# Performance work log

Hardware: AMD Instinct MI355X
Metric: run time of the kernel (lower is better)

## Reference

```python
import jax, jax.numpy as jnp
import numpy as np
from math import sqrt

B, L, H, D = 4, 4096, 8, 64
FACTOR = 5


def setup_inputs():
    key = jax.random.key(0)
    k1, k2, k3, k4 = jax.random.split(key, 4)
    queries = jax.random.normal(k1, (B, L, H, D), dtype=jnp.float32)
    keys = jax.random.normal(k2, (B, L, H, D), dtype=jnp.float32)
    values = jax.random.normal(k3, (B, L, H, D), dtype=jnp.float32)
    sample_k = min(FACTOR * int(np.ceil(np.log(L))), L)  # U_part = 45
    index_sample = jax.random.randint(k4, (L, sample_k), 0, L)
    return {"queries": queries, "keys": keys, "values": values,
            "index_sample": index_sample}


def reference(queries, keys, values, index_sample):
    Bq, L_Q, Hq, Dq = queries.shape
    L_K = keys.shape[1]
    Q = jnp.transpose(queries, (0, 2, 1, 3))  # [B,H,L_Q,D]
    K = jnp.transpose(keys, (0, 2, 1, 3))     # [B,H,L_K,D]
    V = jnp.transpose(values, (0, 2, 1, 3))   # [B,H,L_K,D]
    n_top = min(FACTOR * int(np.ceil(np.log(L_Q))), L_Q)  # u = 45

    # --- _prob_QK: randomly-sampled QK scoring + top-k query selection ---
    K_sample = K[:, :, index_sample, :]                       # [B,H,L_Q,sample_k,D]
    Q_K_sample = jnp.einsum('bhld,bhlkd->bhlk', Q, K_sample)  # [B,H,L_Q,sample_k]
    M = Q_K_sample.max(-1) - Q_K_sample.sum(-1) / L_K         # sparsity measure
    _, M_top = jax.lax.top_k(M, n_top)                        # [B,H,u] query indices
    Q_reduce = jnp.take_along_axis(Q, M_top[..., None], axis=2)  # [B,H,u,D]
    scores = jnp.einsum('bhud,bhkd->bhuk', Q_reduce, K)       # [B,H,u,L_K]

    # scale = 1/sqrt(D) (self.scale is None)
    scores = scores * (1.0 / sqrt(Dq))

    # --- ProbMask (mask_flag=True): causal, key j masked if j > query idx ---
    mask = jnp.arange(L_K)[None, None, None, :] > M_top[..., None]
    scores = jnp.where(mask, -jnp.inf, scores)
    attn = jax.nn.softmax(scores, axis=-1)                    # [B,H,u,L_K]

    # --- initial context (masked case): cumulative sum of V over time ---
    context = jnp.cumsum(V, axis=2)                           # [B,H,L_Q,D]

    # --- scatter attn@V into the selected query positions ---
    upd = jnp.einsum('bhuk,bhkd->bhud', attn, V)              # [B,H,u,D]
    b_idx = jnp.arange(Bq)[:, None, None]
    h_idx = jnp.arange(Hq)[None, :, None]
    context = context.at[b_idx, h_idx, M_top].set(upd)
    return context  # [B,H,L_Q,D], as returned by the torch module
```

## Files before the change

### kernel.cpp

```cpp
#include <hip/hip_runtime.h>

#define NB 4
#define LSEQ 4096
#define NH 8
#define ND 64
#define NSAMP 45
#define NTOP 45
#define ACH 256
#define NCH (LSEQ / ACH)

typedef float f32x4 __attribute__((ext_vector_type(4)));


__global__ __launch_bounds__(256) void fusedA_kernel(
        const int* __restrict__ idxS, int* __restrict__ sortedPack,
        const float* __restrict__ V, float* __restrict__ chunkSums) {
    int blk = blockIdx.x;
    int t = threadIdx.x;
    __shared__ int cnt[256][17];
    __shared__ float part[4][ND];

    if (blk < 16) {
        int l = blk * 256 + t;
        const int* is = idxS + (size_t)l * NSAMP;
        #pragma unroll
        for (int c = 0; c < 16; ++c) cnt[t][c] = 0;
        for (int s = 0; s < NSAMP; ++s) cnt[t][is[s] >> 8] += 1;
        int run = 0;
        #pragma unroll
        for (int c = 0; c < 16; ++c) { int v = cnt[t][c]; cnt[t][c] = run; run += v; }
        for (int s = 0; s < NSAMP; ++s) {
            int idx = is[s];
            int pos = cnt[t][idx >> 8]++;
            sortedPack[(size_t)l * NSAMP + pos] = (idx << 8) | s;
        }
    } else {
        int blk2 = blk - 16;
        int c = blk2 & 15;
        int bh = blk2 >> 4;
        int h = bh & (NH - 1);
        int b = bh >> 3;
        int g = t >> 6, d = t & 63;

        const size_t rstride = (size_t)NH * ND;
        size_t vbase = (size_t)b * LSEQ * rstride + (size_t)h * ND + d;

        int l0 = c * 256 + g * 64;
        float s = 0.0f;
        for (int l = l0; l < l0 + 64; ++l) s += V[vbase + (size_t)l * rstride];

        part[g][d] = s;
        __syncthreads();
        if (t < ND)
            chunkSums[(size_t)blk2 * ND + d] =
                part[0][d] + part[1][d] + part[2][d] + part[3][d];
    }
}

__global__ __launch_bounds__(512, 1) void compute_M_kernel(
        const float* __restrict__ Q,
        const float* __restrict__ K,
        const int* __restrict__ sortedPack,
        float* __restrict__ Mout) {
    int xcd = blockIdx.x & 7;
    int sub = blockIdx.x >> 3;
    int bh  = (xcd << 2) | (sub & 3);
    int lt  = sub >> 2;
    int b = bh >> 3, h = bh & 7;
    int t = threadIdx.x;
    int l0 = (lt << 9) + t;

    __shared__ float Ks[256 * 68];
    __shared__ float Plds[512 * 45];

    f32x4 qa[16];
    {
        const f32x4* qp0 = reinterpret_cast<const f32x4*>(
            Q + (((size_t)b * LSEQ + l0) * NH + h) * ND);
        #pragma unroll
        for (int i = 0; i < 16; ++i) qa[i] = __builtin_nontemporal_load(qp0 + i);
    }

    auto dotQK = [&](const f32x4 (&q4)[16], const float* kr) -> float {
        const f32x4* k4 = reinterpret_cast<const f32x4*>(kr);
        float w[32];
        #pragma unroll
        for (int i = 0; i < 8; ++i) {
            f32x4 a = q4[i], bb = k4[i], c = q4[i + 8], d4 = k4[i + 8];
            w[4 * i + 0] = __fadd_rn(__fmul_rn(a.x, bb.x), __fmul_rn(c.x, d4.x));
            w[4 * i + 1] = __fadd_rn(__fmul_rn(a.y, bb.y), __fmul_rn(c.y, d4.y));
            w[4 * i + 2] = __fadd_rn(__fmul_rn(a.z, bb.z), __fmul_rn(c.z, d4.z));
            w[4 * i + 3] = __fadd_rn(__fmul_rn(a.w, bb.w), __fmul_rn(c.w, d4.w));
        }
        #pragma unroll
        for (int off = 16; off; off >>= 1) {
            #pragma unroll
            for (int i = 0; i < off; ++i) w[i] = __fadd_rn(w[i], w[i + off]);
        }
        return w[0];
    };

    const int* sp0 = sortedPack + (size_t)l0 * NSAMP;
    int ptr0 = 0;
    int pk0 = sp0[0];

    size_t kbh = ((size_t)b * LSEQ * NH + h) * ND;

    for (int c = 0; c < 16; ++c) {
        #pragma unroll
        for (int i = 0; i < 8; ++i) {
            int flat = i * 512 + t;
            int row = flat >> 4, col = flat & 15;
            f32x4 v = *reinterpret_cast<const f32x4*>(
                K + kbh + (size_t)(c * 256 + row) * (NH * ND) + col * 4);
            *reinterpret_cast<f32x4*>(&Ks[row * 68 + col * 4]) = v;
        }
        __syncthreads();

        while ((pk0 >> 16) == c) {
            int r = (pk0 >> 8) & 255;
            int s = pk0 & 255;
            Plds[t * 45 + s] = dotQK(qa, &Ks[r * 68]);
            ++ptr0;
            pk0 = (ptr0 < NSAMP) ? sp0[ptr0] : 0x7fffffff;
        }
        __syncthreads();
    }

    {
        float maxv = -INFINITY, sumv = 0.0f;
        for (int s = 0; s < NSAMP; ++s) {
            float v = Plds[t * 45 + s];
            maxv = fmaxf(maxv, v);
            sumv = __fadd_rn(sumv, v);
        }
        Mout[(size_t)bh * LSEQ + l0] = maxv - sumv * (1.0f / (float)LSEQ);
    }
}

__global__ __launch_bounds__(256) void topk_kernel(
        const float* __restrict__ M, int* __restrict__ Mtop) {
    int bh = blockIdx.x;
    int t = threadIdx.x;
    int wave = t >> 6, lane = t & 63;
    const float* m = M + (size_t)bh * LSEQ;

    float rv[16];
    #pragma unroll
    for (int k = 0; k < 16; ++k) rv[k] = m[t + (k << 8)];

    __shared__ float wv[4];
    __shared__ int   wi[4];
    __shared__ int   winIdx;

    for (int iter = 0; iter < NTOP; ++iter) {
        float bv = -INFINITY; int bi = 0x7fffffff;
        #pragma unroll
        for (int k = 0; k < 16; ++k) {
            float v = rv[k];
            if (v > bv) { bv = v; bi = t + (k << 8); }
        }
        #pragma unroll
        for (int off = 1; off < 64; off <<= 1) {
            float ov = __shfl_xor(bv, off, 64);
            int   oi = __shfl_xor(bi, off, 64);
            if (ov > bv || (ov == bv && oi < bi)) { bv = ov; bi = oi; }
        }
        if (lane == 0) { wv[wave] = bv; wi[wave] = bi; }
        __syncthreads();
        if (t == 0) {
            float cv = wv[0]; int ci = wi[0];
            for (int ww = 1; ww < 4; ++ww) {
                if (wv[ww] > cv || (wv[ww] == cv && wi[ww] < ci)) { cv = wv[ww]; ci = wi[ww]; }
            }
            winIdx = ci;
            Mtop[bh * NTOP + iter] = ci;
        }
        __syncthreads();
        int widx = winIdx;
        #pragma unroll
        for (int k = 0; k < 16; ++k)
            if (widx == t + (k << 8)) rv[k] = -INFINITY;
        __syncthreads();
    }
}

__global__ __launch_bounds__(256, 1) void attn_partial_kernel(
        const float* __restrict__ Q, const float* __restrict__ K,
        const float* __restrict__ V, const int* __restrict__ Mtop,
        float* __restrict__ part) {
    int bh = blockIdx.x >> 4;
    int c  = blockIdx.x & 15;
    int b = bh >> 3, h = bh & 7;
    int t = threadIdx.x;
    int w = t >> 6, lane = t & 63;
    int jj = lane >> 4, dq = lane & 15;

    __shared__ float Qs[NTOP * ND];
    __shared__ int   posS[NTOP];
    __shared__ float Vs[64][68];
    __shared__ float Pw[4][64];

    size_t base = ((size_t)b * LSEQ * NH + h) * ND;

    if (t < NTOP) posS[t] = Mtop[bh * NTOP + t];
    __syncthreads();
    for (int idx = t; idx < NTOP * 16; idx += 256) {
        int u = idx >> 4, cg = idx & 15;
        f32x4 v = *reinterpret_cast<const f32x4*>(
            Q + base + (size_t)posS[u] * (NH * ND) + cg * 4);
        *reinterpret_cast<f32x4*>(&Qs[u * ND + cg * 4]) = v;
    }

    f32x4 o[12];
    float mreg[12], sreg[12];
    #pragma unroll
    for (int qi = 0; qi < 12; ++qi) {
        o[qi] = 0.0f; mreg[qi] = -INFINITY; sreg[qi] = 0.0f;
    }

    for (int tt = 0; tt < ACH / 64; ++tt) {
        int tile0 = c * ACH + tt * 64;
        __syncthreads();
        #pragma unroll
        for (int i = 0; i < 4; ++i) {
            int flat = i * 256 + t;
            int r = flat >> 4, cg = flat & 15;
            f32x4 v = *reinterpret_cast<const f32x4*>(
                V + base + (size_t)(tile0 + r) * (NH * ND) + cg * 4);
            *reinterpret_cast<f32x4*>(&Vs[r][cg * 4]) = v;
        }
        __syncthreads();

        f32x4 kreg[16];
        #pragma unroll
        for (int i = 0; i < 16; ++i)
            kreg[i] = *reinterpret_cast<const f32x4*>(
                K + base + (size_t)(tile0 + lane) * (NH * ND) + i * 4);

        #pragma unroll
        for (int qi = 0; qi < 12; ++qi) {
            int u = w + 4 * qi;
            if (u >= NTOP) continue;
            int pu = posS[u];
            if (pu < tile0) continue;

            float a0 = 0, a1 = 0, a2 = 0, a3 = 0;
            #pragma unroll
            for (int di = 0; di < 16; ++di) {
                f32x4 qv = *reinterpret_cast<const f32x4*>(&Qs[u * ND + di * 4]);
                a0 = fmaf(qv.x, kreg[di].x, a0);
                a1 = fmaf(qv.y, kreg[di].y, a1);
                a2 = fmaf(qv.z, kreg[di].z, a2);
                a3 = fmaf(qv.w, kreg[di].w, a3);
            }
            float sc = ((a0 + a1) + (a2 + a3)) * 0.125f;
            if (tile0 + lane > pu) sc = -INFINITY;

            float tmax = sc;
            #pragma unroll
            for (int off = 1; off < 64; off <<= 1)
                tmax = fmaxf(tmax, __shfl_xor(tmax, off, 64));
            float mold = mreg[qi];
            float mnew = fmaxf(mold, tmax);
            float alpha = __expf(mold - mnew);
            float e = __expf(sc - mnew);
            float esum = e;
            #pragma unroll
            for (int off = 1; off < 64; off <<= 1)
                esum += __shfl_xor(esum, off, 64);
            sreg[qi] = sreg[qi] * alpha + esum;
            mreg[qi] = mnew;
            Pw[w][lane] = e;
            o[qi] *= alpha;
            #pragma unroll
            for (int i = 0; i < 16; ++i) {
                float pe = Pw[w][i * 4 + jj];
                f32x4 vv = *reinterpret_cast<const f32x4*>(&Vs[i * 4 + jj][dq * 4]);
                o[qi] += vv * pe;
            }
        }
    }

    #pragma unroll
    for (int qi = 0; qi < 12; ++qi) {
        int u = w + 4 * qi;
        if (u >= NTOP) continue;
        if (posS[u] < c * ACH) continue;
        f32x4 oo = o[qi];
        #pragma unroll
        for (int off = 16; off <= 32; off <<= 1) {
            oo.x += __shfl_xor(oo.x, off, 64);
            oo.y += __shfl_xor(oo.y, off, 64);
            oo.z += __shfl_xor(oo.z, off, 64);
            oo.w += __shfl_xor(oo.w, off, 64);
        }
        size_t pb = ((size_t)(bh * NTOP + u) * NCH + c) * 72;
        if (lane < 16)
            *reinterpret_cast<f32x4*>(&part[pb + 4 + dq * 4]) = oo;
        if (lane == 0) { part[pb] = mreg[qi]; part[pb + 1] = sreg[qi]; }
    }
}

__global__ __launch_bounds__(256) void attn_merge_kernel(
        const float* __restrict__ part, const int* __restrict__ Mtop,
        float* __restrict__ ctx) {
    int j = blockIdx.x * 4 + (threadIdx.x >> 6);
    int lane = threadIdx.x & 63;
    int bh = j / NTOP, u = j - bh * NTOP;
    int pos = Mtop[bh * NTOP + u];
    int cmax = pos >> 8;
    size_t pb0 = (size_t)(bh * NTOP + u) * NCH * 72;
    float m = -INFINITY;
    for (int cc = 0; cc <= cmax; ++cc)
        m = fmaxf(m, part[pb0 + (size_t)cc * 72]);
    float S = 0.0f, oacc = 0.0f;
    for (int cc = 0; cc <= cmax; ++cc) {
        float mc = part[pb0 + (size_t)cc * 72];
        float sc = part[pb0 + (size_t)cc * 72 + 1];
        float wgt = __expf(mc - m);
        S = fmaf(sc, wgt, S);
        oacc = fmaf(part[pb0 + (size_t)cc * 72 + 4 + lane], wgt, oacc);
    }
    ctx[(size_t)j * ND + lane] = oacc / S;
}

__global__ __launch_bounds__(256) void cumsumCS_kernel(
        const float* __restrict__ V, const float* __restrict__ chunkSums,
        const int* __restrict__ Mtop, const float* __restrict__ ctx,
        float* __restrict__ out, int doScatter) {
    int blk = blockIdx.x;
    int c = blk & 15;
    int bh = blk >> 4;
    int h = bh & (NH - 1);
    int b = bh >> 3;
    int g = threadIdx.x >> 6, d = threadIdx.x & 63;
    int t = threadIdx.x;

    const size_t rstride = (size_t)NH * ND;
    size_t vbase = (size_t)b * LSEQ * rstride + (size_t)h * ND + d;

    float run = 0.0f;
    for (int cc = 0; cc < c; ++cc)
        run += chunkSums[((size_t)bh * 16 + cc) * ND + d];

    int l0 = c * 256 + g * 64;
    float s = 0.0f;
    for (int l = l0; l < l0 + 64; ++l) s += V[vbase + (size_t)l * rstride];
    __shared__ float part[4][ND];
    part[g][d] = s;
    __syncthreads();
    for (int gg = 0; gg < g; ++gg) run += part[gg][d];

    size_t obase = (size_t)bh * LSEQ * ND + d;
    for (int l = l0; l < l0 + 64; ++l) {
        run += V[vbase + (size_t)l * rstride];
        out[obase + (size_t)l * ND] = run;
    }

    if (!doScatter) return;
    __syncthreads();
    for (int idx = t; idx < NTOP * ND; idx += 256) {
        int u = idx >> 6, d2 = idx & 63;
        int pos = Mtop[bh * NTOP + u];
        if ((pos >> 8) == c)
            out[((size_t)bh * LSEQ + pos) * ND + d2] =
                ctx[(size_t)(bh * NTOP + u) * ND + d2];
    }
}

#define TJ 64
__global__ __launch_bounds__(256) void attn_rows_kernel(
        const float* __restrict__ Q,
        const float* __restrict__ K,
        const float* __restrict__ V,
        const int* __restrict__ Mtop,
        float* __restrict__ out) {
    int x = blockIdx.x;
    int xcd = x & 7;
    int slot = x >> 3;
    int grp = slot / NTOP;
    int u = slot % NTOP;
    int bh = grp * 8 + xcd;
    int h = bh & (NH - 1);
    int b = bh >> 3;
    int pos = Mtop[bh * NTOP + u];
    int n = pos + 1;
    int t = threadIdx.x;
    int r = t >> 2, qt = t & 3;

    __shared__ float Ks[TJ][65];
    __shared__ float Vs[TJ][65];
    __shared__ float red[256];

    const size_t rstride = (size_t)NH * ND;
    size_t base = (size_t)b * LSEQ * rstride + (size_t)h * ND;

    float qreg[16];
    const float* qrow = Q + base + (size_t)pos * rstride + qt * 16;
    #pragma unroll
    for (int i = 0; i < 16; i += 4) {
        float4 v4 = *reinterpret_cast<const float4*>(qrow + i);
        qreg[i] = v4.x; qreg[i + 1] = v4.y; qreg[i + 2] = v4.z; qreg[i + 3] = v4.w;
    }

    float m = -INFINITY, s = 0.0f;
    float o[16];
    #pragma unroll
    for (int dd = 0; dd < 16; ++dd) o[dd] = 0.0f;

    int ntiles = (n + TJ - 1) / TJ;
    for (int tt = 0; tt < ntiles; ++tt) {
        int j0 = tt * TJ;
        __syncthreads();
        #pragma unroll
        for (int i = 0; i < 4; ++i) {
            int u16 = t + i * 256;
            int rr = u16 >> 4, cc = u16 & 15;
            int j = j0 + rr;
            int jc = (j < n) ? j : (n - 1);
            const float* rowk = K + base + (size_t)jc * rstride;
            float4 kv = *reinterpret_cast<const float4*>(rowk + cc * 4);
            Ks[rr][cc * 4 + 0] = kv.x; Ks[rr][cc * 4 + 1] = kv.y;
            Ks[rr][cc * 4 + 2] = kv.z; Ks[rr][cc * 4 + 3] = kv.w;
            const float* rowv = V + base + (size_t)jc * rstride;
            float4 vv = *reinterpret_cast<const float4*>(rowv + cc * 4);
            Vs[rr][cc * 4 + 0] = vv.x; Vs[rr][cc * 4 + 1] = vv.y;
            Vs[rr][cc * 4 + 2] = vv.z; Vs[rr][cc * 4 + 3] = vv.w;
        }
        __syncthreads();

        int j = j0 + r;
        float acc = 0.0f;
        #pragma unroll
        for (int dd = 0; dd < 16; ++dd)
            acc = fmaf(qreg[dd], Ks[r][qt * 16 + dd], acc);
        acc += __shfl_xor(acc, 1, 64);
        acc += __shfl_xor(acc, 2, 64);

        if (j < n) {
            float sc = acc * 0.125f;
            if (sc > m) {
                float alpha = __expf(m - sc);
                s *= alpha;
                #pragma unroll
                for (int dd = 0; dd < 16; ++dd) o[dd] *= alpha;
                m = sc;
            }
            float e = __expf(sc - m);
            s += e;
            #pragma unroll
            for (int dd = 0; dd < 16; ++dd)
                o[dd] = fmaf(e, Vs[r][qt * 16 + dd], o[dd]);
        }
    }
    __syncthreads();

    red[t] = m; __syncthreads();
    for (int sft = 128; sft; sft >>= 1) {
        if (t < sft) red[t] = fmaxf(red[t], red[t + sft]);
        __syncthreads();
    }
    float mstar = red[0]; __syncthreads();
    float a = __expf(m - mstar);

    red[t] = s * a; __syncthreads();
    for (int sft = 128; sft; sft >>= 1) {
        if (t < sft) red[t] += red[t + sft];
        __syncthreads();
    }
    float S = red[0]; __syncthreads();

    float* OB = &Ks[0][0];
    #pragma unroll
    for (int dd = 0; dd < 16; ++dd) OB[t * 16 + dd] = o[dd] * a;
    __syncthreads();

    if (t < ND) {
        int qtt = t >> 4, dd = t & 15;
        float tot = 0.0f;
        for (int k = 0; k < 64; ++k) tot += OB[(4 * k + qtt) * 16 + dd];
        out[((size_t)bh * LSEQ + pos) * ND + t] = tot / S;
    }
}

extern "C" void kernel_launch(void* const* d_in, const int* in_sizes, int n_in,
                              void* d_out, int out_size, void* d_ws, size_t ws_size,
                              hipStream_t stream) {
    const float* Q = (const float*)d_in[0];
    const float* K = (const float*)d_in[1];
    const float* V = (const float*)d_in[2];
    const int* idxS = (const int*)d_in[3];
    float* out = (float*)d_out;

    float* Mbuf = (float*)d_out;
    int*   sortedPack = (int*)((char*)d_out + (1 << 20));
    float* part = (float*)((char*)d_out + (2 << 20));
    int*   Mtop = (int*)d_ws;
    float* chunkSums = (float*)((char*)d_ws + 8192);
    float* ctx = (float*)((char*)d_ws + 8192 + 131072);
    size_t wsMid = 8192 + 131072 + (size_t)NB * NH * NTOP * ND * 4;

    fusedA_kernel<<<528, 256, 0, stream>>>(idxS, sortedPack, V, chunkSums);
    compute_M_kernel<<<256, 512, 0, stream>>>(Q, K, sortedPack, Mbuf);
    topk_kernel<<<NB * NH, 256, 0, stream>>>(Mbuf, Mtop);

    if (ws_size >= wsMid) {
        attn_partial_kernel<<<NB * NH * NCH, 256, 0, stream>>>(Q, K, V, Mtop, part);
        attn_merge_kernel<<<NB * NH * NTOP / 4, 256, 0, stream>>>(part, Mtop, ctx);
        cumsumCS_kernel<<<NB * NH * 16, 256, 0, stream>>>(V, chunkSums, Mtop, ctx, out, 1);
    } else {
        cumsumCS_kernel<<<NB * NH * 16, 256, 0, stream>>>(V, chunkSums, Mtop, ctx, out, 0);
        attn_rows_kernel<<<NB * NH * NTOP, 256, 0, stream>>>(Q, K, V, Mtop, out);
    }
}
```

Before: 424.3 us.

## Split sample dots across 1024 threads and fuse attention merge into cumsum scatter

compute_M now runs 1024 threads per block: two threads per query, each handling an interleaved half of the sorted sample list. It stages K in 512-row tiles and keeps a running max and sum in registers instead of writing every dot product to LDS, then combines the two halves through shared memory. The separate merge kernel is removed, and the scatter step of the cumsum kernel now merges the per-chunk softmax partials directly, which drops one launch and the ctx round trip. The partials buffer moves into the workspace, so the fast path now needs a much larger workspace; if it is not available, the slower row-wise fallback runs.

```diff
diff --git a/kernel.cpp b/kernel.cpp
--- a/kernel.cpp
+++ b/kernel.cpp
@@ -8,12 +8,13 @@
 #define NTOP 45
 #define ACH 256
 #define NCH (LSEQ / ACH)
+#define SENT 0x7fffffff
 
 typedef float f32x4 __attribute__((ext_vector_type(4)));
 
 
 __global__ __launch_bounds__(256) void fusedA_kernel(
-        const int* __restrict__ idxS, int* __restrict__ sortedPack,
+        const int* __restrict__ idxS, int* __restrict__ sortedAB,
         const float* __restrict__ V, float* __restrict__ chunkSums) {
     int blk = blockIdx.x;
     int t = threadIdx.x;
@@ -29,10 +30,12 @@
         int run = 0;
         #pragma unroll
         for (int c = 0; c < 16; ++c) { int v = cnt[t][c]; cnt[t][c] = run; run += v; }
+        int* ab = sortedAB + (size_t)l * 48;
+        ab[23] = SENT; ab[46] = SENT; ab[47] = SENT;
         for (int s = 0; s < NSAMP; ++s) {
             int idx = is[s];
-            int pos = cnt[t][idx >> 8]++;
-            sortedPack[(size_t)l * NSAMP + pos] = (idx << 8) | s;
+            int p = cnt[t][idx >> 8]++;
+            ab[(p & 1) * 24 + (p >> 1)] = (idx << 8) | s;
         }
     } else {
         int blk2 = blk - 16;
@@ -57,10 +60,10 @@
     }
 }
 
-__global__ __launch_bounds__(512, 1) void compute_M_kernel(
+__global__ __launch_bounds__(1024, 1) void compute_M_kernel(
         const float* __restrict__ Q,
         const float* __restrict__ K,
-        const int* __restrict__ sortedPack,
+        const int* __restrict__ sortedAB,
         float* __restrict__ Mout) {
     int xcd = blockIdx.x & 7;
     int sub = blockIdx.x >> 3;
@@ -68,17 +71,20 @@
     int lt  = sub >> 2;
     int b = bh >> 3, h = bh & 7;
     int t = threadIdx.x;
-    int l0 = (lt << 9) + t;
-
-    __shared__ float Ks[256 * 68];
-    __shared__ float Plds[512 * 45];
+    int lloc = t & 511;
+    int par  = t >> 9;
+    int l = (lt << 9) | lloc;
+
+    __shared__ float Ks[512 * 68];
+    __shared__ float redM[1024];
+    __shared__ float redS[1024];
 
     f32x4 qa[16];
     {
-        const f32x4* qp0 = reinterpret_cast<const f32x4*>(
-            Q + (((size_t)b * LSEQ + l0) * NH + h) * ND);
-        #pragma unroll
-        for (int i = 0; i < 16; ++i) qa[i] = __builtin_nontemporal_load(qp0 + i);
+        const f32x4* qp = reinterpret_cast<const f32x4*>(
+            Q + (((size_t)b * LSEQ + l) * NH + h) * ND);
+        #pragma unroll
+        for (int i = 0; i < 16; ++i) qa[i] = __builtin_nontemporal_load(qp + i);
     }
 
     auto dotQK = [&](const f32x4 (&q4)[16], const float* kr) -> float {
@@ -100,41 +106,46 @@
         return w[0];
     };
 
-    const int* sp0 = sortedPack + (size_t)l0 * NSAMP;
-    int ptr0 = 0;
-    int pk0 = sp0[0];
+    const int* sp = sortedAB + (size_t)l * 48 + par * 24;
+    int ptr = 1;
+    int pk = sp[0];
+    int pknext = sp[1];
 
     size_t kbh = ((size_t)b * LSEQ * NH + h) * ND;
 
-    for (int c = 0; c < 16; ++c) {
+    float maxv = -INFINITY;
+    float sumv = 0.0f;
+
+    for (int c2 = 0; c2 < 8; ++c2) {
         #pragma unroll
         for (int i = 0; i < 8; ++i) {
-            int flat = i * 512 + t;
+            int flat = i * 1024 + t;
             int row = flat >> 4, col = flat & 15;
             f32x4 v = *reinterpret_cast<const f32x4*>(
-                K + kbh + (size_t)(c * 256 + row) * (NH * ND) + col * 4);
+                K + kbh + (size_t)(c2 * 512 + row) * (NH * ND) + col * 4);
             *reinterpret_cast<f32x4*>(&Ks[row * 68 + col * 4]) = v;
         }
         __syncthreads();
 
-        while ((pk0 >> 16) == c) {
-            int r = (pk0 >> 8) & 255;
-            int s = pk0 & 255;
-            Plds[t * 45 + s] = dotQK(qa, &Ks[r * 68]);
-            ++ptr0;
-            pk0 = (ptr0 < NSAMP) ? sp0[ptr0] : 0x7fffffff;
-        }
-        __syncthreads();
-    }
-
-    {
-        float maxv = -INFINITY, sumv = 0.0f;
-        for (int s = 0; s < NSAMP; ++s) {
-            float v = Plds[t * 45 + s];
-            maxv = fmaxf(maxv, v);
-            sumv = __fadd_rn(sumv, v);
-        }
-        Mout[(size_t)bh * LSEQ + l0] = maxv - sumv * (1.0f / (float)LSEQ);
+        while ((pk >> 17) == c2) {
+            int r = (pk >> 8) & 511;
+            ++ptr;
+            int pk2 = sp[ptr];
+            float p = dotQK(qa, &Ks[r * 68]);
+            maxv = fmaxf(maxv, p);
+            sumv = __fadd_rn(sumv, p);
+            pk = pknext;
+            pknext = pk2;
+        }
+        __syncthreads();
+    }
+
+    redM[t] = maxv; redS[t] = sumv;
+    __syncthreads();
+    if (t < 512) {
+        float m = fmaxf(redM[t], redM[t + 512]);
+        float s = __fadd_rn(redS[t], redS[t + 512]);
+        Mout[(size_t)bh * LSEQ + ((lt << 9) | t)] = m - s * (1.0f / (float)LSEQ);
     }
 }
 
@@ -302,32 +313,9 @@
     }
 }
 
-__global__ __launch_bounds__(256) void attn_merge_kernel(
-        const float* __restrict__ part, const int* __restrict__ Mtop,
-        float* __restrict__ ctx) {
-    int j = blockIdx.x * 4 + (threadIdx.x >> 6);
-    int lane = threadIdx.x & 63;
-    int bh = j / NTOP, u = j - bh * NTOP;
-    int pos = Mtop[bh * NTOP + u];
-    int cmax = pos >> 8;
-    size_t pb0 = (size_t)(bh * NTOP + u) * NCH * 72;
-    float m = -INFINITY;
-    for (int cc = 0; cc <= cmax; ++cc)
-        m = fmaxf(m, part[pb0 + (size_t)cc * 72]);
-    float S = 0.0f, oacc = 0.0f;
-    for (int cc = 0; cc <= cmax; ++cc) {
-        float mc = part[pb0 + (size_t)cc * 72];
-        float sc = part[pb0 + (size_t)cc * 72 + 1];
-        float wgt = __expf(mc - m);
-        S = fmaf(sc, wgt, S);
-        oacc = fmaf(part[pb0 + (size_t)cc * 72 + 4 + lane], wgt, oacc);
-    }
-    ctx[(size_t)j * ND + lane] = oacc / S;
-}
-
 __global__ __launch_bounds__(256) void cumsumCS_kernel(
         const float* __restrict__ V, const float* __restrict__ chunkSums,
-        const int* __restrict__ Mtop, const float* __restrict__ ctx,
+        const int* __restrict__ Mtop, const float* __restrict__ part,
         float* __restrict__ out, int doScatter) {
     int blk = blockIdx.x;
     int c = blk & 15;
@@ -347,10 +335,10 @@
     int l0 = c * 256 + g * 64;
     float s = 0.0f;
     for (int l = l0; l < l0 + 64; ++l) s += V[vbase + (size_t)l * rstride];
-    __shared__ float part[4][ND];
-    part[g][d] = s;
+    __shared__ float cpart[4][ND];
+    cpart[g][d] = s;
     __syncthreads();
-    for (int gg = 0; gg < g; ++gg) run += part[gg][d];
+    for (int gg = 0; gg < g; ++gg) run += cpart[gg][d];
 
     size_t obase = (size_t)bh * LSEQ * ND + d;
     for (int l = l0; l < l0 + 64; ++l) {
@@ -360,12 +348,23 @@
 
     if (!doScatter) return;
     __syncthreads();
-    for (int idx = t; idx < NTOP * ND; idx += 256) {
-        int u = idx >> 6, d2 = idx & 63;
+    int w = t >> 6, lane = t & 63;
+    for (int u = w; u < NTOP; u += 4) {
         int pos = Mtop[bh * NTOP + u];
-        if ((pos >> 8) == c)
-            out[((size_t)bh * LSEQ + pos) * ND + d2] =
-                ctx[(size_t)(bh * NTOP + u) * ND + d2];
+        if ((pos >> 8) != c) continue;
+        size_t pb0 = (size_t)(bh * NTOP + u) * NCH * 72;
+        float mm = -INFINITY;
+        for (int cc = 0; cc <= c; ++cc)
+            mm = fmaxf(mm, part[pb0 + (size_t)cc * 72]);
+        float S = 0.0f, oacc = 0.0f;
+        for (int cc = 0; cc <= c; ++cc) {
+            float mc = part[pb0 + (size_t)cc * 72];
+            float sc = part[pb0 + (size_t)cc * 72 + 1];
+            float wgt = __expf(mc - mm);
+            S = fmaf(sc, wgt, S);
+            oacc = fmaf(part[pb0 + (size_t)cc * 72 + 4 + lane], wgt, oacc);
+        }
+        out[((size_t)bh * LSEQ + pos) * ND + lane] = oacc / S;
     }
 }
 
@@ -494,23 +493,21 @@
     float* out = (float*)d_out;
 
     float* Mbuf = (float*)d_out;
-    int*   sortedPack = (int*)((char*)d_out + (1 << 20));
-    float* part = (float*)((char*)d_out + (2 << 20));
+    int*   sortedAB = (int*)((char*)d_out + (1 << 20));
     int*   Mtop = (int*)d_ws;
     float* chunkSums = (float*)((char*)d_ws + 8192);
-    float* ctx = (float*)((char*)d_ws + 8192 + 131072);
-    size_t wsMid = 8192 + 131072 + (size_t)NB * NH * NTOP * ND * 4;
-
-    fusedA_kernel<<<528, 256, 0, stream>>>(idxS, sortedPack, V, chunkSums);
-    compute_M_kernel<<<256, 512, 0, stream>>>(Q, K, sortedPack, Mbuf);
+    float* part = (float*)((char*)d_ws + 139264);
+    size_t wsNeed = 139264 + (size_t)NB * NH * NTOP * NCH * 72 * 4;
+
+    fusedA_kernel<<<528, 256, 0, stream>>>(idxS, sortedAB, V, chunkSums);
+    compute_M_kernel<<<256, 1024, 0, stream>>>(Q, K, sortedAB, Mbuf);
     topk_kernel<<<NB * NH, 256, 0, stream>>>(Mbuf, Mtop);
 
-    if (ws_size >= wsMid) {
+    if (ws_size >= wsNeed) {
         attn_partial_kernel<<<NB * NH * NCH, 256, 0, stream>>>(Q, K, V, Mtop, part);
-        attn_merge_kernel<<<NB * NH * NTOP / 4, 256, 0, stream>>>(part, Mtop, ctx);
-        cumsumCS_kernel<<<NB * NH * 16, 256, 0, stream>>>(V, chunkSums, Mtop, ctx, out, 1);
+        cumsumCS_kernel<<<NB * NH * 16, 256, 0, stream>>>(V, chunkSums, Mtop, part, out, 1);
     } else {
-        cumsumCS_kernel<<<NB * NH * 16, 256, 0, stream>>>(V, chunkSums, Mtop, ctx, out, 0);
+        cumsumCS_kernel<<<NB * NH * 16, 256, 0, stream>>>(V, chunkSums, Mtop, part, out, 0);
         attn_rows_kernel<<<NB * NH * NTOP, 256, 0, stream>>>(Q, K, V, Mtop, out);
     }
 }
```

After: 444.8 us. +4.8%, slower.
